# Performance work log

Measured on AMD Instinct MI355X. Metric: run time of the kernel, lower is better.

## Reference

```python
import jax, jax.numpy as jnp
import numpy as np

N = 100000   # nodes
E = 1600000  # edges (avg degree 16)
D = 128      # in_dim == hidden_dim (required by residual + shared BN)
G = 64       # graphs in the batch
EPS = 1e-5   # BatchNorm eps


def setup_inputs() -> dict:
    key = jax.random.key(0)
    ks = jax.random.split(key, 10)
    h = jax.random.normal(ks[0], (N, D), jnp.float32)
    src = jax.random.randint(ks[1], (E,), 0, N)
    dst = jax.random.randint(ks[2], (E,), 0, N)
    graph_ids = jnp.sort(jax.random.randint(ks[3], (N,), 0, G))
    s = 1.0 / np.sqrt(D)
    W1 = jax.random.uniform(ks[4], (D, D), jnp.float32, -s, s)
    b1 = jnp.zeros((D,), jnp.float32)
    W2 = jax.random.uniform(ks[5], (D, D), jnp.float32, -s, s)
    b2 = jnp.zeros((D,), jnp.float32)
    gate_W = jax.random.uniform(ks[6], (D, 1), jnp.float32, -s, s)
    gate_b = jnp.zeros((1,), jnp.float32)
    gamma = jnp.ones((D,), jnp.float32)
    beta = jnp.zeros((D,), jnp.float32)
    return {"h": h, "src": src, "dst": dst, "graph_ids": graph_ids,
            "num_graphs": G, "W1": W1, "b1": b1, "W2": W2, "b2": b2,
            "gate_W": gate_W, "gate_b": gate_b, "gamma": gamma, "beta": beta}


def reference(h, src, dst, graph_ids, num_graphs, W1, b1, W2, b2, gate_W, gate_b, gamma, beta):
    n = h.shape[0]

    # dgl.mean_nodes: per-graph mean of initial features
    node_counts = jnp.clip(jax.ops.segment_sum(jnp.ones((n,), h.dtype), graph_ids, num_graphs), 1.0)
    init_avg_h = jax.ops.segment_sum(h, graph_ids, num_graphs) / node_counts[:, None]

    # training-mode BatchNorm1d with shared gamma/beta (same bn module used twice)
    def bn(x):
        m = jnp.mean(x, axis=0)
        v = jnp.mean(jnp.square(x - m), axis=0)  # biased variance (torch BN)
        return (x - m) * jax.lax.rsqrt(v + EPS) * gamma + beta

    ones_e = jnp.ones(src.shape[0], h.dtype)
    deg_out = jnp.clip(jax.ops.segment_sum(ones_e, src, n), 1.0)  # out-degree of src
    deg_in = jnp.clip(jax.ops.segment_sum(ones_e, dst, n), 1.0)   # in-degree of dst
    inv_sqrt_out = jax.lax.rsqrt(deg_out)[:, None]
    inv_sqrt_in = jax.lax.rsqrt(deg_in)[:, None]

    # DGL GraphConv, norm='both': D_dst^{-1/2} A (D_src^{-1/2} x) W + b
    def graph_conv(x, W, b):
        xs = x * inv_sqrt_out
        agg = jax.ops.segment_sum(xs[src], dst, n)  # SpMM: gather src, scatter-add at dst
        return (agg * inv_sqrt_in) @ W + b

    h1 = h + jax.nn.relu(graph_conv(bn(h), W1, b1))
    h2 = h1 + jax.nn.relu(graph_conv(bn(h1), W2, b2))

    # GlobalAttentionPooling: per-graph softmax over gate scores, weighted sum of h2
    gate = h2 @ gate_W + gate_b  # [N, 1]
    gmax = jax.ops.segment_max(gate, graph_ids, num_graphs)
    e = jnp.exp(gate - gmax[graph_ids])
    denom = jax.ops.segment_sum(e, graph_ids, num_graphs)
    alpha = e / denom[graph_ids]
    hg = jax.ops.segment_sum(alpha * h2, graph_ids, num_graphs)  # [G, D]

    return hg, init_avg_h
```

## Files before the change

### kernel.cpp

```cpp
#include <hip/hip_runtime.h>
#include <math.h>

#define N_NODES 100000
#define N_EDGES 1600000
#define DIM     128
#define NG      64
#define BN_EPS  1e-5f
#define NB      98
#define HRANGE  12500
#define NSLICE  16
#define ESLICE  (N_EDGES / NSLICE)
#define NBLK_CONV 1563
#define SB      128
#define NSB     782

typedef __attribute__((ext_vector_type(8))) short bf16x8;
typedef __attribute__((ext_vector_type(4))) float f32x4;

__device__ __forceinline__ unsigned short f2bf(float f) {
  unsigned b = __float_as_uint(f);
  unsigned r = (b + 0x7FFFu + ((b >> 16) & 1u)) >> 16;
  return (unsigned short)r;
}

__launch_bounds__(1024)
__global__ void k_histO(const int* __restrict__ src, int* __restrict__ cntO) {
  __shared__ int histo[HRANGE];
  int t = threadIdx.x;
  int range = blockIdx.x >> 3, blk = blockIdx.x & 7;
  int lo = range * HRANGE;
  for (int j = t; j < HRANGE; j += 1024) histo[j] = 0;
  __syncthreads();
  const int SLICE = N_EDGES / 8;
  const int4* sp = (const int4*)(src + blk * SLICE);
  const int n4 = SLICE / 4;
  for (int q = t; q < n4; q += 1024) {
    int4 v = sp[q];
    unsigned a = (unsigned)(v.x - lo), b = (unsigned)(v.y - lo);
    unsigned c = (unsigned)(v.z - lo), d = (unsigned)(v.w - lo);
    if (a < (unsigned)HRANGE) atomicAdd(&histo[a], 1);
    if (b < (unsigned)HRANGE) atomicAdd(&histo[b], 1);
    if (c < (unsigned)HRANGE) atomicAdd(&histo[c], 1);
    if (d < (unsigned)HRANGE) atomicAdd(&histo[d], 1);
  }
  __syncthreads();
  for (int j = t; j < HRANGE; j += 1024) {
    int v = histo[j];
    if (v) atomicAdd(&cntO[lo + j], v);
  }
}

__launch_bounds__(1024)
__global__ void k_histD(const int* __restrict__ dst, int* __restrict__ cnt_slice) {
  __shared__ int histo[HRANGE];
  int t = threadIdx.x;
  int range = blockIdx.x >> 4, slice = blockIdx.x & 15;
  int lo = range * HRANGE;
  for (int j = t; j < HRANGE; j += 1024) histo[j] = 0;
  __syncthreads();
  const int4* dp = (const int4*)(dst + slice * ESLICE);
  for (int q = t; q < ESLICE / 4; q += 1024) {
    int4 v = dp[q];
    unsigned a = (unsigned)(v.x - lo), b = (unsigned)(v.y - lo);
    unsigned c = (unsigned)(v.z - lo), d = (unsigned)(v.w - lo);
    if (a < (unsigned)HRANGE) atomicAdd(&histo[a], 1);
    if (b < (unsigned)HRANGE) atomicAdd(&histo[b], 1);
    if (c < (unsigned)HRANGE) atomicAdd(&histo[c], 1);
    if (d < (unsigned)HRANGE) atomicAdd(&histo[d], 1);
  }
  __syncthreads();
  for (int j = t; j < HRANGE; j += 1024)
    cnt_slice[(size_t)slice * N_NODES + lo + j] = histo[j];
}

__global__ void k_scan_part(const int* __restrict__ cnt_slice, int* __restrict__ cnt,
                            int* __restrict__ bsum) {
  int b = blockIdx.x, t = threadIdx.x;
  int base = b * 1024 + t * 4;
  int tot = 0;
#pragma unroll
  for (int j = 0; j < 4; ++j) {
    int i = base + j;
    if (i < N_NODES) {
      int c = 0;
#pragma unroll
      for (int s = 0; s < NSLICE; ++s) c += cnt_slice[(size_t)s * N_NODES + i];
      cnt[i] = c;
      tot += c;
    }
  }
  __shared__ int red[256];
  red[t] = tot; __syncthreads();
  for (int w = 128; w; w >>= 1) { if (t < w) red[t] += red[t + w]; __syncthreads(); }
  if (t == 0) bsum[b] = red[0];
}

__global__ void k_scan_mid(const int* __restrict__ bsum, int* __restrict__ boff,
                           int* __restrict__ rowstart) {
  int t = threadIdx.x;
  __shared__ int sh[128];
  int own = (t < NB) ? bsum[t] : 0;
  sh[t] = own;
  __syncthreads();
  for (int off = 1; off < 128; off <<= 1) {
    int v = (t >= off) ? sh[t - off] : 0;
    __syncthreads();
    sh[t] += v;
    __syncthreads();
  }
  if (t < NB) boff[t] = sh[t] - own;
  if (t == NB - 1) rowstart[N_NODES] = sh[t];
}

__global__ void k_scan_fin(const int* __restrict__ cnt, const int* __restrict__ boff,
                           int* __restrict__ rowstart) {
  int b = blockIdx.x, t = threadIdx.x;
  int base = b * 1024 + t * 4;
  int v0 = 0, v1 = 0, v2 = 0, v3 = 0;
  if (base + 0 < N_NODES) v0 = cnt[base + 0];
  if (base + 1 < N_NODES) v1 = cnt[base + 1];
  if (base + 2 < N_NODES) v2 = cnt[base + 2];
  if (base + 3 < N_NODES) v3 = cnt[base + 3];
  int tsum = v0 + v1 + v2 + v3;
  __shared__ int sh[256];
  sh[t] = tsum;
  __syncthreads();
  for (int off = 1; off < 256; off <<= 1) {
    int v = (t >= off) ? sh[t - off] : 0;
    __syncthreads();
    sh[t] += v;
    __syncthreads();
  }
  int run = boff[b] + sh[t] - tsum;
  if (base + 0 < N_NODES) rowstart[base + 0] = run; run += v0;
  if (base + 1 < N_NODES) rowstart[base + 1] = run; run += v1;
  if (base + 2 < N_NODES) rowstart[base + 2] = run; run += v2;
  if (base + 3 < N_NODES) rowstart[base + 3] = run;
}

__global__ void k_sliceoff(int* __restrict__ cnt_slice) {
  int i = blockIdx.x * 256 + threadIdx.x;
  if (i < N_NODES) {
    int run = 0;
#pragma unroll
    for (int s = 0; s < NSLICE; ++s) {
      int v = cnt_slice[(size_t)s * N_NODES + i];
      cnt_slice[(size_t)s * N_NODES + i] = run;
      run += v;
    }
  }
}

__launch_bounds__(1024)
__global__ void k_scatter_slice(const int* __restrict__ src, const int* __restrict__ dst,
                                const int* __restrict__ rowstart,
                                const int* __restrict__ cnt_slice, int* __restrict__ csr) {
  __shared__ int cur[HRANGE];
  int t = threadIdx.x;
  int range = blockIdx.x >> 4, slice = blockIdx.x & 15;
  int lo = range * HRANGE;
  for (int j = t; j < HRANGE; j += 1024)
    cur[j] = rowstart[lo + j] + cnt_slice[(size_t)slice * N_NODES + lo + j];
  __syncthreads();
  const int4* dp = (const int4*)(dst + slice * ESLICE);
  const int4* sp = (const int4*)(src + slice * ESLICE);
  for (int q = t; q < ESLICE / 4; q += 1024) {
    int4 d = dp[q];
    int4 s = sp[q];
    unsigned o;
    o = (unsigned)(d.x - lo); if (o < (unsigned)HRANGE) { int p = atomicAdd(&cur[o], 1); csr[p] = s.x; }
    o = (unsigned)(d.y - lo); if (o < (unsigned)HRANGE) { int p = atomicAdd(&cur[o], 1); csr[p] = s.y; }
    o = (unsigned)(d.z - lo); if (o < (unsigned)HRANGE) { int p = atomicAdd(&cur[o], 1); csr[p] = s.z; }
    o = (unsigned)(d.w - lo); if (o < (unsigned)HRANGE) { int p = atomicAdd(&cur[o], 1); csr[p] = s.w; }
  }
}

__global__ void k_starts_fill(const int* __restrict__ gid, int* __restrict__ starts) {
  int i = blockIdx.x * blockDim.x + threadIdx.x;
  if (i >= N_NODES) return;
  int gi = gid[i];
  if (i == 0) {
    for (int g = 0; g <= gi; ++g) starts[g] = 0;
  } else {
    int gp = gid[i - 1];
    if (gp != gi) for (int g = gp + 1; g <= gi; ++g) starts[g] = i;
  }
  if (i == N_NODES - 1) {
    for (int g = gi + 1; g <= NG; ++g) starts[g] = N_NODES;
  }
}

__launch_bounds__(256)
__global__ void k_stats1(const float* __restrict__ x, const int* __restrict__ gid,
                         float* __restrict__ sums, float* __restrict__ initavg) {
  __shared__ float ls[8][DIM];
  __shared__ float ls2[8][DIM];
  __shared__ float lseg[4][8][DIM];
  int t = threadIdx.x;
  int col4 = (t & 31) * 4, rg = t >> 5;
  for (int i = t; i < 4 * 8 * DIM; i += 256) ((float*)lseg)[i] = 0.f;
  int base = blockIdx.x * SB;
  int rend = min(base + SB, N_NODES);
  int g0 = gid[base];
  int gl = gid[rend - 1];
  __syncthreads();
  float4 s = {0.f,0.f,0.f,0.f}, s2 = {0.f,0.f,0.f,0.f};
  float4 acc = {0.f,0.f,0.f,0.f};
  if (g0 == gl) {
    for (int r = base + rg; r < rend; r += 8) {
      float4 v = *(const float4*)&x[(size_t)r * DIM + col4];
      s.x += v.x; s.y += v.y; s.z += v.z; s.w += v.w;
      s2.x += v.x*v.x; s2.y += v.y*v.y; s2.z += v.z*v.z; s2.w += v.w*v.w;
      acc.x += v.x; acc.y += v.y; acc.z += v.z; acc.w += v.w;
    }
    lseg[0][rg][col4+0] = acc.x; lseg[0][rg][col4+1] = acc.y;
    lseg[0][rg][col4+2] = acc.z; lseg[0][rg][col4+3] = acc.w;
  } else {
    int curg = g0;
    for (int r = base + rg; r < rend; r += 8) {
      float4 v = *(const float4*)&x[(size_t)r * DIM + col4];
      s.x += v.x; s.y += v.y; s.z += v.z; s.w += v.w;
      s2.x += v.x*v.x; s2.y += v.y*v.y; s2.z += v.z*v.z; s2.w += v.w*v.w;
      int g = gid[r];
      if (g != curg) {
        int slot = curg - g0;
        if (slot < 4) {
          lseg[slot][rg][col4+0] = acc.x; lseg[slot][rg][col4+1] = acc.y;
          lseg[slot][rg][col4+2] = acc.z; lseg[slot][rg][col4+3] = acc.w;
        } else {
          atomicAdd(&initavg[curg * DIM + col4+0], acc.x);
          atomicAdd(&initavg[curg * DIM + col4+1], acc.y);
          atomicAdd(&initavg[curg * DIM + col4+2], acc.z);
          atomicAdd(&initavg[curg * DIM + col4+3], acc.w);
        }
        acc.x = acc.y = acc.z = acc.w = 0.f;
        curg = g;
      }
      acc.x += v.x; acc.y += v.y; acc.z += v.z; acc.w += v.w;
    }
    int slot = curg - g0;
    if (slot < 4) {
      lseg[slot][rg][col4+0] = acc.x; lseg[slot][rg][col4+1] = acc.y;
      lseg[slot][rg][col4+2] = acc.z; lseg[slot][rg][col4+3] = acc.w;
    } else {
      atomicAdd(&initavg[curg * DIM + col4+0], acc.x);
      atomicAdd(&initavg[curg * DIM + col4+1], acc.y);
      atomicAdd(&initavg[curg * DIM + col4+2], acc.z);
      atomicAdd(&initavg[curg * DIM + col4+3], acc.w);
    }
  }
  *(float4*)&ls[rg][col4] = s;
  *(float4*)&ls2[rg][col4] = s2;
  __syncthreads();
  if (t < DIM) {
    float a = 0.f, b = 0.f;
#pragma unroll
    for (int j = 0; j < 8; ++j) { a += ls[j][t]; b += ls2[j][t]; }
    atomicAdd(&sums[t], a);
    atomicAdd(&sums[DIM + t], b);
#pragma unroll
    for (int slot = 0; slot < 4; ++slot) {
      float v = 0.f;
#pragma unroll
      for (int j = 0; j < 8; ++j) v += lseg[slot][j][t];
      int g = g0 + slot;
      if (g < NG && v != 0.f) atomicAdd(&initavg[g * DIM + t], v);
    }
  }
}

__global__ void k_avg_div(const int* __restrict__ starts, float* __restrict__ outp) {
  int g = blockIdx.x, d = threadIdx.x;
  float cnt = fmaxf((float)(starts[g + 1] - starts[g]), 1.0f);
  outp[g * DIM + d] /= cnt;
}

__global__ void k_colred(const float* __restrict__ psum, const float* __restrict__ psq,
                         float* __restrict__ sums) {
  int c = blockIdx.x, t = threadIdx.x;
  __shared__ float r1[256], r2[256];
  float a = 0.f, b = 0.f;
  for (int j = t; j < NBLK_CONV; j += 256) {
    a += psum[(size_t)c * NBLK_CONV + j];
    b += psq[(size_t)c * NBLK_CONV + j];
  }
  r1[t] = a; r2[t] = b; __syncthreads();
  for (int w = 128; w; w >>= 1) { if (t < w) { r1[t] += r1[t + w]; r2[t] += r2[t + w]; } __syncthreads(); }
  if (t == 0) { sums[c] = r1[0]; sums[DIM + c] = r2[0]; }
}

__launch_bounds__(256)
__global__ void k_bnx(const float* __restrict__ x, const float* __restrict__ sums,
                      const float* __restrict__ gamma, const float* __restrict__ beta,
                      const int* __restrict__ cntO, unsigned short* __restrict__ xb) {
  int idx = blockIdx.x * 256 + threadIdx.x;
  int row = idx >> 5, c4 = (idx & 31) * 4;
  float4 sm = *(const float4*)&sums[c4];
  float4 sq = *(const float4*)&sums[DIM + c4];
  float4 ga = *(const float4*)&gamma[c4];
  float4 be = *(const float4*)&beta[c4];
  const float inv = 1.0f / N_NODES;
  float4 sc, sh;
  {
    float m = sm.x * inv, va = sq.x * inv - m * m;
    sc.x = rsqrtf(fmaxf(va, 0.f) + BN_EPS) * ga.x; sh.x = be.x - m * sc.x;
    m = sm.y * inv; va = sq.y * inv - m * m;
    sc.y = rsqrtf(fmaxf(va, 0.f) + BN_EPS) * ga.y; sh.y = be.y - m * sc.y;
    m = sm.z * inv; va = sq.z * inv - m * m;
    sc.z = rsqrtf(fmaxf(va, 0.f) + BN_EPS) * ga.z; sh.z = be.z - m * sc.z;
    m = sm.w * inv; va = sq.w * inv - m * m;
    sc.w = rsqrtf(fmaxf(va, 0.f) + BN_EPS) * ga.w; sh.w = be.w - m * sc.w;
  }
  float4 v = *(const float4*)&x[(size_t)row * DIM + c4];
  float f = rsqrtf(fmaxf((float)cntO[row], 1.0f));
  ushort4 o;
  o.x = f2bf((v.x * sc.x + sh.x) * f);
  o.y = f2bf((v.y * sc.y + sh.y) * f);
  o.z = f2bf((v.z * sc.z + sh.z) * f);
  o.w = f2bf((v.w * sc.w + sh.w) * f);
  *(ushort4*)&xb[(size_t)row * DIM + c4] = o;
}

__global__ void k_prepW(const float* __restrict__ W1, const float* __restrict__ W2,
                        unsigned short* __restrict__ WbT1, unsigned short* __restrict__ WbT2) {
  int idx = blockIdx.x * 256 + threadIdx.x;
  int which = idx >> 14;
  int i = idx & 16383;
  int k = i >> 7, c = i & 127;
  const float* W = which ? W2 : W1;
  unsigned short* O = which ? WbT2 : WbT1;
  O[c * DIM + k] = f2bf(W[k * DIM + c]);
}

__launch_bounds__(256, 8)
__global__ void k_spmm_pull(const unsigned short* __restrict__ xb, const int* __restrict__ csr,
                            const int* __restrict__ rowstart, unsigned short* __restrict__ aggb) {
  int row = blockIdx.x * 4 + threadIdx.y;
  int l = threadIdx.x;
  int half = l >> 5, l32 = l & 31;
  int s = rowstart[row], e = rowstart[row + 1];
  float4 acc = {0.f, 0.f, 0.f, 0.f};
  const size_t coff = (size_t)l32 * 4;
  int i = s + half;
  for (; i + 6 < e; i += 8) {
    int s0 = csr[i], s1 = csr[i + 2], s2 = csr[i + 4], s3 = csr[i + 6];
    uint2 w0 = *(const uint2*)&xb[(size_t)s0 * DIM + coff];
    uint2 w1 = *(const uint2*)&xb[(size_t)s1 * DIM + coff];
    uint2 w2 = *(const uint2*)&xb[(size_t)s2 * DIM + coff];
    uint2 w3 = *(const uint2*)&xb[(size_t)s3 * DIM + coff];
    acc.x += __uint_as_float(w0.x << 16) + __uint_as_float(w1.x << 16)
           + __uint_as_float(w2.x << 16) + __uint_as_float(w3.x << 16);
    acc.y += __uint_as_float(w0.x & 0xFFFF0000u) + __uint_as_float(w1.x & 0xFFFF0000u)
           + __uint_as_float(w2.x & 0xFFFF0000u) + __uint_as_float(w3.x & 0xFFFF0000u);
    acc.z += __uint_as_float(w0.y << 16) + __uint_as_float(w1.y << 16)
           + __uint_as_float(w2.y << 16) + __uint_as_float(w3.y << 16);
    acc.w += __uint_as_float(w0.y & 0xFFFF0000u) + __uint_as_float(w1.y & 0xFFFF0000u)
           + __uint_as_float(w2.y & 0xFFFF0000u) + __uint_as_float(w3.y & 0xFFFF0000u);
  }
  for (; i < e; i += 2) {
    int s0 = csr[i];
    uint2 w0 = *(const uint2*)&xb[(size_t)s0 * DIM + coff];
    acc.x += __uint_as_float(w0.x << 16);
    acc.y += __uint_as_float(w0.x & 0xFFFF0000u);
    acc.z += __uint_as_float(w0.y << 16);
    acc.w += __uint_as_float(w0.y & 0xFFFF0000u);
  }
  acc.x += __shfl_xor(acc.x, 32);
  acc.y += __shfl_xor(acc.y, 32);
  acc.z += __shfl_xor(acc.z, 32);
  acc.w += __shfl_xor(acc.w, 32);
  if (half == 0) {
    float isi = rsqrtf(fmaxf((float)(e - s), 1.0f));
    ushort4 o;
    o.x = f2bf(acc.x * isi);
    o.y = f2bf(acc.y * isi);
    o.z = f2bf(acc.z * isi);
    o.w = f2bf(acc.w * isi);
    *(ushort4*)&aggb[(size_t)row * DIM + l32 * 4] = o;
  }
}

__launch_bounds__(256)
__global__ void k_conv(const unsigned short* __restrict__ aggb,
                       const unsigned short* __restrict__ WbT,
                       const float* __restrict__ bias, const float* __restrict__ hres,
                       float* __restrict__ outp,
                       const float* __restrict__ gWp, const float* __restrict__ gbp,
                       float* __restrict__ gatep,
                       float* __restrict__ psum, float* __restrict__ psq) {
  __shared__ unsigned short As[64 * 136];
  __shared__ unsigned short Ws[128 * 136];
  __shared__ float gsh[64];
  float* Of = (float*)Ws;
  int t = threadIdx.x;
  int row0 = blockIdx.x * 64;

  if (gatep && t < 64) gsh[t] = 0.f;

  for (int i = t; i < 1024; i += 256) {
    int r = i >> 4, q = i & 15;
    int row = row0 + r;
    int4 v = {0, 0, 0, 0};
    if (row < N_NODES) v = *(const int4*)&aggb[(size_t)row * DIM + q * 8];
    *(int4*)&As[r * 136 + q * 8] = v;
  }
  for (int i = t; i < 2048; i += 256) {
    int c = i >> 4, q = i & 15;
    *(int4*)&Ws[c * 136 + q * 8] = *(const int4*)&WbT[(size_t)c * DIM + q * 8];
  }
  __syncthreads();

  int wid = t >> 6, l = t & 63;
  int wr = wid >> 1, wc = wid & 1;
  int lr = l & 15, lq = l >> 4;
  f32x4 acc[2][4] = {};
  const unsigned short* Ab = &As[(wr * 32 + lr) * 136 + lq * 8];
  const unsigned short* Bb = &Ws[(wc * 64 + lr) * 136 + lq * 8];
#pragma unroll
  for (int kk = 0; kk < 4; ++kk) {
    bf16x8 a0 = *(const bf16x8*)(Ab + kk * 32);
    bf16x8 a1 = *(const bf16x8*)(Ab + 16 * 136 + kk * 32);
    bf16x8 b0 = *(const bf16x8*)(Bb + kk * 32);
    bf16x8 b1 = *(const bf16x8*)(Bb + 16 * 136 + kk * 32);
    bf16x8 b2 = *(const bf16x8*)(Bb + 32 * 136 + kk * 32);
    bf16x8 b3 = *(const bf16x8*)(Bb + 48 * 136 + kk * 32);
    acc[0][0] = __builtin_amdgcn_mfma_f32_16x16x32_bf16(a0, b0, acc[0][0], 0, 0, 0);
    acc[0][1] = __builtin_amdgcn_mfma_f32_16x16x32_bf16(a0, b1, acc[0][1], 0, 0, 0);
    acc[0][2] = __builtin_amdgcn_mfma_f32_16x16x32_bf16(a0, b2, acc[0][2], 0, 0, 0);
    acc[0][3] = __builtin_amdgcn_mfma_f32_16x16x32_bf16(a0, b3, acc[0][3], 0, 0, 0);
    acc[1][0] = __builtin_amdgcn_mfma_f32_16x16x32_bf16(a1, b0, acc[1][0], 0, 0, 0);
    acc[1][1] = __builtin_amdgcn_mfma_f32_16x16x32_bf16(a1, b1, acc[1][1], 0, 0, 0);
    acc[1][2] = __builtin_amdgcn_mfma_f32_16x16x32_bf16(a1, b2, acc[1][2], 0, 0, 0);
    acc[1][3] = __builtin_amdgcn_mfma_f32_16x16x32_bf16(a1, b3, acc[1][3], 0, 0, 0);
  }
  __syncthreads();

#pragma unroll
  for (int rt = 0; rt < 2; ++rt) {
#pragma unroll
    for (int ct = 0; ct < 4; ++ct) {
      int rr = wr * 32 + rt * 16 + lq * 4;
      int cc = wc * 64 + ct * 16 + lr;
#pragma unroll
      for (int i = 0; i < 4; ++i)
        Of[(rr + i) * 132 + cc] = acc[rt][ct][i];
    }
  }
  __syncthreads();

  float st[4] = {0.f, 0.f, 0.f, 0.f}, st2[4] = {0.f, 0.f, 0.f, 0.f};
#pragma unroll
  for (int i = 0; i < 8; ++i) {
    int fi = t + i * 256;
    int r = fi >> 5, c4 = (fi & 31) * 4;
    int row = row0 + r;
    if (row < N_NODES) {
      float4 o  = *(float4*)&Of[r * 132 + c4];
      float4 bv = *(const float4*)&bias[c4];
      float4 hv = *(const float4*)&hres[(size_t)row * DIM + c4];
      float4 y = {hv.x + fmaxf(o.x + bv.x, 0.f), hv.y + fmaxf(o.y + bv.y, 0.f),
                  hv.z + fmaxf(o.z + bv.z, 0.f), hv.w + fmaxf(o.w + bv.w, 0.f)};
      *(float4*)&outp[(size_t)row * DIM + c4] = y;
      if (gatep) {
        float4 gw = *(const float4*)&gWp[c4];
        atomicAdd(&gsh[r], y.x * gw.x + y.y * gw.y + y.z * gw.z + y.w * gw.w);
      }
      if (psum) {
        st[0] += y.x; st[1] += y.y; st[2] += y.z; st[3] += y.w;
        st2[0] += y.x*y.x; st2[1] += y.y*y.y; st2[2] += y.z*y.z; st2[3] += y.w*y.w;
      }
    }
  }
  if (gatep) {
    __syncthreads();
    int row = row0 + t;
    if (t < 64 && row < N_NODES) gatep[row] = gsh[t] + gbp[0];
  }
  if (psum) {
    float* sls  = (float*)As;
    float* sls2 = sls + 8 * DIM;
    int rg = t >> 5, c4 = (t & 31) * 4;
    __syncthreads();
#pragma unroll
    for (int i = 0; i < 4; ++i) {
      sls[rg * DIM + c4 + i]  = st[i];
      sls2[rg * DIM + c4 + i] = st2[i];
    }
    __syncthreads();
    if (t < DIM) {
      float a = 0.f, b = 0.f;
#pragma unroll
      for (int j = 0; j < 8; ++j) { a += sls[j * DIM + t]; b += sls2[j * DIM + t]; }
      psum[(size_t)t * NBLK_CONV + blockIdx.x] = a;
      psq[(size_t)t * NBLK_CONV + blockIdx.x]  = b;
    }
  }
}

__global__ void k_gstats(const float* __restrict__ gate, const int* __restrict__ starts,
                         float* __restrict__ gmax, float* __restrict__ gden) {
  int g = blockIdx.x;
  int s = starts[g], e = starts[g + 1];
  int t = threadIdx.x;
  __shared__ float red[256];
  float m = -INFINITY;
  for (int i = s + t; i < e; i += 256) m = fmaxf(m, gate[i]);
  red[t] = m; __syncthreads();
  for (int w = 128; w; w >>= 1) { if (t < w) red[t] = fmaxf(red[t], red[t + w]); __syncthreads(); }
  float mg = red[0]; __syncthreads();
  float ssum = 0.f;
  for (int i = s + t; i < e; i += 256) ssum += expf(gate[i] - mg);
  red[t] = ssum; __syncthreads();
  for (int w = 128; w; w >>= 1) { if (t < w) red[t] += red[t + w]; __syncthreads(); }
  if (t == 0) { gmax[g] = mg; gden[g] = red[0]; }
}

__global__ void k_pool(const float* __restrict__ h2, const float* __restrict__ gate,
                       const int* __restrict__ starts, const float* __restrict__ gmax,
                       const float* __restrict__ gden, float* __restrict__ outp) {
  int g = blockIdx.x >> 3, part = blockIdx.x & 7;
  int s = starts[g], e = starts[g + 1];
  int d = threadIdx.x;
  float mg = gmax[g];
  float dn = gden[g];
  float invden = dn > 0.f ? 1.0f / dn : 0.f;
  float acc = 0.f;
  for (int i = s + part; i < e; i += 8) {
    float w = expf(gate[i] - mg) * invden;
    acc += w * h2[(size_t)i * DIM + d];
  }
  atomicAdd(&outp[g * DIM + d], acc);
}

extern "C" void kernel_launch(void* const* d_in, const int* in_sizes, int n_in,
                              void* d_out, int out_size, void* d_ws, size_t ws_size,
                              hipStream_t stream) {
  const float* h    = (const float*)d_in[0];
  const int*   src  = (const int*)d_in[1];
  const int*   dst  = (const int*)d_in[2];
  const int*   gid  = (const int*)d_in[3];
  const float* W1   = (const float*)d_in[5];
  const float* b1   = (const float*)d_in[6];
  const float* W2   = (const float*)d_in[7];
  const float* b2   = (const float*)d_in[8];
  const float* gW   = (const float*)d_in[9];
  const float* gb   = (const float*)d_in[10];
  const float* gamma= (const float*)d_in[11];
  const float* beta = (const float*)d_in[12];
  float* out = (float*)d_out;

  char* ws = (char*)d_ws;
  float* h12     = (float*)ws; ws += (size_t)N_NODES * DIM * 4;
  unsigned short* xb   = (unsigned short*)ws; ws += (size_t)N_NODES * DIM * 2;
  unsigned short* aggb = (unsigned short*)ws; ws += (size_t)N_NODES * DIM * 2;
  int*   csr     = (int*)ws;   ws += (size_t)N_EDGES * 4;
  int*   cnt_slice = (int*)ws; ws += (size_t)NSLICE * N_NODES * 4;
  float* psum    = (float*)ws; ws += (size_t)DIM * NBLK_CONV * 4;
  float* psq     = (float*)ws; ws += (size_t)DIM * NBLK_CONV * 4;
  unsigned short* WbT1 = (unsigned short*)ws; ws += DIM * DIM * 2;
  unsigned short* WbT2 = (unsigned short*)ws; ws += DIM * DIM * 2;
  int*   rowstart= (int*)ws;   ws += (N_NODES + 1) * 4;
  int*   cnt     = (int*)ws;   ws += N_NODES * 4;
  int*   cntO    = (int*)ws;   ws += N_NODES * 4;
  float* gate    = (float*)ws; ws += N_NODES * 4;
  float* sums    = (float*)ws; ws += 2 * DIM * 4;
  float* gmax    = (float*)ws; ws += NG * 4;
  float* gden    = (float*)ws; ws += NG * 4;
  int*   starts  = (int*)ws;   ws += (NG + 1) * 4;
  int*   bsum    = (int*)ws;   ws += NB * 4;
  int*   boff    = (int*)ws;   ws += NB * 4;

  hipMemsetAsync(cntO,  0, N_NODES * 4, stream);
  hipMemsetAsync(sums,  0, 2 * DIM * 4, stream);
  hipMemsetAsync(d_out, 0, (size_t)out_size * 4, stream);

  k_histO<<<64, 1024, 0, stream>>>(src, cntO);
  k_histD<<<8 * NSLICE, 1024, 0, stream>>>(dst, cnt_slice);
  k_scan_part<<<NB, 256, 0, stream>>>(cnt_slice, cnt, bsum);
  k_scan_mid<<<1, 128, 0, stream>>>(bsum, boff, rowstart);
  k_scan_fin<<<NB, 256, 0, stream>>>(cnt, boff, rowstart);
  k_sliceoff<<<(N_NODES + 255) / 256, 256, 0, stream>>>(cnt_slice);
  k_scatter_slice<<<8 * NSLICE, 1024, 0, stream>>>(src, dst, rowstart, cnt_slice, csr);
  k_starts_fill<<<(N_NODES + 255) / 256, 256, 0, stream>>>(gid, starts);
  k_prepW<<<128, 256, 0, stream>>>(W1, W2, WbT1, WbT2);

  k_stats1<<<NSB, 256, 0, stream>>>(h, gid, sums, out + NG * DIM);
  k_avg_div<<<NG, DIM, 0, stream>>>(starts, out + NG * DIM);
  k_bnx<<<N_NODES * 32 / 256, 256, 0, stream>>>(h, sums, gamma, beta, cntO, xb);
  k_spmm_pull<<<N_NODES / 4, dim3(64, 4), 0, stream>>>(xb, csr, rowstart, aggb);
  k_conv<<<NBLK_CONV, 256, 0, stream>>>(aggb, WbT1, b1, h, h12,
                                        nullptr, nullptr, nullptr, psum, psq);

  k_colred<<<DIM, 256, 0, stream>>>(psum, psq, sums);
  k_bnx<<<N_NODES * 32 / 256, 256, 0, stream>>>(h12, sums, gamma, beta, cntO, xb);
  k_spmm_pull<<<N_NODES / 4, dim3(64, 4), 0, stream>>>(xb, csr, rowstart, aggb);
  k_conv<<<NBLK_CONV, 256, 0, stream>>>(aggb, WbT2, b2, h12, h12,
                                        gW, gb, gate, nullptr, nullptr);

  k_gstats<<<NG, 256, 0, stream>>>(gate, starts, gmax, gden);
  k_pool<<<NG * 8, DIM, 0, stream>>>(h12, gate, starts, gmax, gden, out);
}
```

Baseline: 432.3 us.

## Double edge slices, fuse slice-offset scan into scan_part, unroll SpMM gather by 16

Raises the number of edge slices from 16 to 32 so the histogram and scatter kernels launch 256 blocks instead of 64 or 128, spreading CSR construction across more CUs. The per-slice exclusive offset computation is folded into k_scan_part, which removes the separate k_sliceoff launch and one extra pass over cnt_slice. The SpMM pull loop gains a 16-edge unrolled stage that keeps more independent gathers in flight. Costs are a cnt_slice array twice as large, each block rereading the same edge data, and higher register use in the SpMM kernel.

Result: faster. 418.0 us (-3.3%).

```diff
diff --git a/kernel.cpp b/kernel.cpp
--- a/kernel.cpp
+++ b/kernel.cpp
@@ -8,7 +8,7 @@
 #define BN_EPS  1e-5f
 #define NB      98
 #define HRANGE  12500
-#define NSLICE  16
+#define NSLICE  32
 #define ESLICE  (N_EDGES / NSLICE)
 #define NBLK_CONV 1563
 #define SB      128
@@ -27,14 +27,12 @@
 __global__ void k_histO(const int* __restrict__ src, int* __restrict__ cntO) {
   __shared__ int histo[HRANGE];
   int t = threadIdx.x;
-  int range = blockIdx.x >> 3, blk = blockIdx.x & 7;
+  int range = blockIdx.x >> 5, blk = blockIdx.x & 31;
   int lo = range * HRANGE;
   for (int j = t; j < HRANGE; j += 1024) histo[j] = 0;
   __syncthreads();
-  const int SLICE = N_EDGES / 8;
-  const int4* sp = (const int4*)(src + blk * SLICE);
-  const int n4 = SLICE / 4;
-  for (int q = t; q < n4; q += 1024) {
+  const int4* sp = (const int4*)(src + blk * ESLICE);
+  for (int q = t; q < ESLICE / 4; q += 1024) {
     int4 v = sp[q];
     unsigned a = (unsigned)(v.x - lo), b = (unsigned)(v.y - lo);
     unsigned c = (unsigned)(v.z - lo), d = (unsigned)(v.w - lo);
@@ -54,7 +52,7 @@
 __global__ void k_histD(const int* __restrict__ dst, int* __restrict__ cnt_slice) {
   __shared__ int histo[HRANGE];
   int t = threadIdx.x;
-  int range = blockIdx.x >> 4, slice = blockIdx.x & 15;
+  int range = blockIdx.x >> 5, slice = blockIdx.x & 31;
   int lo = range * HRANGE;
   for (int j = t; j < HRANGE; j += 1024) histo[j] = 0;
   __syncthreads();
@@ -73,7 +71,7 @@
     cnt_slice[(size_t)slice * N_NODES + lo + j] = histo[j];
 }
 
-__global__ void k_scan_part(const int* __restrict__ cnt_slice, int* __restrict__ cnt,
+__global__ void k_scan_part(int* __restrict__ cnt_slice, int* __restrict__ cnt,
                             int* __restrict__ bsum) {
   int b = blockIdx.x, t = threadIdx.x;
   int base = b * 1024 + t * 4;
@@ -82,11 +80,15 @@
   for (int j = 0; j < 4; ++j) {
     int i = base + j;
     if (i < N_NODES) {
-      int c = 0;
-#pragma unroll
-      for (int s = 0; s < NSLICE; ++s) c += cnt_slice[(size_t)s * N_NODES + i];
-      cnt[i] = c;
-      tot += c;
+      int run = 0;
+#pragma unroll
+      for (int s = 0; s < NSLICE; ++s) {
+        int v = cnt_slice[(size_t)s * N_NODES + i];
+        cnt_slice[(size_t)s * N_NODES + i] = run;
+        run += v;
+      }
+      cnt[i] = run;
+      tot += run;
     }
   }
   __shared__ int red[256];
@@ -138,26 +140,13 @@
   if (base + 3 < N_NODES) rowstart[base + 3] = run;
 }
 
-__global__ void k_sliceoff(int* __restrict__ cnt_slice) {
-  int i = blockIdx.x * 256 + threadIdx.x;
-  if (i < N_NODES) {
-    int run = 0;
-#pragma unroll
-    for (int s = 0; s < NSLICE; ++s) {
-      int v = cnt_slice[(size_t)s * N_NODES + i];
-      cnt_slice[(size_t)s * N_NODES + i] = run;
-      run += v;
-    }
-  }
-}
-
 __launch_bounds__(1024)
 __global__ void k_scatter_slice(const int* __restrict__ src, const int* __restrict__ dst,
                                 const int* __restrict__ rowstart,
                                 const int* __restrict__ cnt_slice, int* __restrict__ csr) {
   __shared__ int cur[HRANGE];
   int t = threadIdx.x;
-  int range = blockIdx.x >> 4, slice = blockIdx.x & 15;
+  int range = blockIdx.x >> 5, slice = blockIdx.x & 31;
   int lo = range * HRANGE;
   for (int j = t; j < HRANGE; j += 1024)
     cur[j] = rowstart[lo + j] + cnt_slice[(size_t)slice * N_NODES + lo + j];
@@ -342,6 +331,34 @@
   float4 acc = {0.f, 0.f, 0.f, 0.f};
   const size_t coff = (size_t)l32 * 4;
   int i = s + half;
+  for (; i + 14 < e; i += 16) {
+    int s0 = csr[i],      s1 = csr[i + 2],  s2 = csr[i + 4],  s3 = csr[i + 6];
+    int s4 = csr[i + 8],  s5 = csr[i + 10], s6 = csr[i + 12], s7 = csr[i + 14];
+    uint2 w0 = *(const uint2*)&xb[(size_t)s0 * DIM + coff];
+    uint2 w1 = *(const uint2*)&xb[(size_t)s1 * DIM + coff];
+    uint2 w2 = *(const uint2*)&xb[(size_t)s2 * DIM + coff];
+    uint2 w3 = *(const uint2*)&xb[(size_t)s3 * DIM + coff];
+    uint2 w4 = *(const uint2*)&xb[(size_t)s4 * DIM + coff];
+    uint2 w5 = *(const uint2*)&xb[(size_t)s5 * DIM + coff];
+    uint2 w6 = *(const uint2*)&xb[(size_t)s6 * DIM + coff];
+    uint2 w7 = *(const uint2*)&xb[(size_t)s7 * DIM + coff];
+    acc.x += (__uint_as_float(w0.x << 16) + __uint_as_float(w1.x << 16))
+           + (__uint_as_float(w2.x << 16) + __uint_as_float(w3.x << 16))
+           + (__uint_as_float(w4.x << 16) + __uint_as_float(w5.x << 16))
+           + (__uint_as_float(w6.x << 16) + __uint_as_float(w7.x << 16));
+    acc.y += (__uint_as_float(w0.x & 0xFFFF0000u) + __uint_as_float(w1.x & 0xFFFF0000u))
+           + (__uint_as_float(w2.x & 0xFFFF0000u) + __uint_as_float(w3.x & 0xFFFF0000u))
+           + (__uint_as_float(w4.x & 0xFFFF0000u) + __uint_as_float(w5.x & 0xFFFF0000u))
+           + (__uint_as_float(w6.x & 0xFFFF0000u) + __uint_as_float(w7.x & 0xFFFF0000u));
+    acc.z += (__uint_as_float(w0.y << 16) + __uint_as_float(w1.y << 16))
+           + (__uint_as_float(w2.y << 16) + __uint_as_float(w3.y << 16))
+           + (__uint_as_float(w4.y << 16) + __uint_as_float(w5.y << 16))
+           + (__uint_as_float(w6.y << 16) + __uint_as_float(w7.y << 16));
+    acc.w += (__uint_as_float(w0.y & 0xFFFF0000u) + __uint_as_float(w1.y & 0xFFFF0000u))
+           + (__uint_as_float(w2.y & 0xFFFF0000u) + __uint_as_float(w3.y & 0xFFFF0000u))
+           + (__uint_as_float(w4.y & 0xFFFF0000u) + __uint_as_float(w5.y & 0xFFFF0000u))
+           + (__uint_as_float(w6.y & 0xFFFF0000u) + __uint_as_float(w7.y & 0xFFFF0000u));
+  }
   for (; i + 6 < e; i += 8) {
     int s0 = csr[i], s1 = csr[i + 2], s2 = csr[i + 4], s3 = csr[i + 6];
     uint2 w0 = *(const uint2*)&xb[(size_t)s0 * DIM + coff];
@@ -574,13 +591,12 @@
   hipMemsetAsync(sums,  0, 2 * DIM * 4, stream);
   hipMemsetAsync(d_out, 0, (size_t)out_size * 4, stream);
 
-  k_histO<<<64, 1024, 0, stream>>>(src, cntO);
-  k_histD<<<8 * NSLICE, 1024, 0, stream>>>(dst, cnt_slice);
+  k_histO<<<256, 1024, 0, stream>>>(src, cntO);
+  k_histD<<<256, 1024, 0, stream>>>(dst, cnt_slice);
   k_scan_part<<<NB, 256, 0, stream>>>(cnt_slice, cnt, bsum);
   k_scan_mid<<<1, 128, 0, stream>>>(bsum, boff, rowstart);
   k_scan_fin<<<NB, 256, 0, stream>>>(cnt, boff, rowstart);
-  k_sliceoff<<<(N_NODES + 255) / 256, 256, 0, stream>>>(cnt_slice);
-  k_scatter_slice<<<8 * NSLICE, 1024, 0, stream>>>(src, dst, rowstart, cnt_slice, csr);
+  k_scatter_slice<<<256, 1024, 0, stream>>>(src, dst, rowstart, cnt_slice, csr);
   k_starts_fill<<<(N_NODES + 255) / 256, 256, 0, stream>>>(gid, starts);
   k_prepW<<<128, 256, 0, stream>>>(W1, W2, WbT1, WbT2);
 
```
